# Performance work log

Measured on AMD Instinct MI355X. Metric: run time of the kernel, lower is better.

Reference implementation:

```python
import jax, jax.numpy as jnp
import numpy as np

N_NODES = 100000

def _sage_conv(x, src, dst, w_l, b_l, w_r):
    # PyG SAGEConv (mean aggr): out = lin_l(mean_j x_j) + lin_r(x_i)
    msg = x[src]                                             # [E, d] gather
    agg = jax.ops.segment_sum(msg, dst, num_segments=N_NODES)
    deg = jax.ops.segment_sum(jnp.ones((src.shape[0],), x.dtype), dst,
                              num_segments=N_NODES)
    mean = agg / jnp.maximum(deg, 1.0)[:, None]
    return mean @ w_l.T + b_l + x @ w_r.T


def setup_inputs() -> dict:
    key = jax.random.key(0)
    ks = jax.random.split(key, 9)
    d_in, d_h, d_out = 128, 128, 4
    E = 1600000
    x = jax.random.normal(ks[0], (N_NODES, d_in), dtype=jnp.float32)
    edge_index = jax.random.randint(ks[1], (2, E), 0, N_NODES, dtype=jnp.int32)
    s = lambda k, shp, fan: jax.random.normal(k, shp, jnp.float32) / np.sqrt(fan)
    return {
        "x": x,
        "edge_index": edge_index,
        "w1_l": s(ks[2], (d_h, d_in), d_in),
        "b1_l": jnp.zeros((d_h,), jnp.float32),
        "w1_r": s(ks[3], (d_h, d_in), d_in),
        "w2_l": s(ks[4], (d_h, d_h), d_h),
        "b2_l": jnp.zeros((d_h,), jnp.float32),
        "w2_r": s(ks[5], (d_h, d_h), d_h),
        "w_out": s(ks[6], (d_out, d_h), d_h),
        "b_out": jnp.zeros((d_out,), jnp.float32),
    }


def reference(x, edge_index, w1_l, b1_l, w1_r, w2_l, b2_l, w2_r, w_out, b_out):
    src, dst = edge_index[0], edge_index[1]
    h = jax.nn.relu(_sage_conv(x, src, dst, w1_l, b1_l, w1_r))
    h = jax.nn.relu(_sage_conv(h, src, dst, w2_l, b2_l, w2_r))
    return h @ w_out.T + b_out
```

## Files before the change

### kernel.cpp

```cpp
#include <hip/hip_runtime.h>

constexpr int D = 128;
constexpr int BSHIFT = 10;
constexpr int BNODES = 1 << BSHIFT;
constexpr int NBUCK_MAX = 128;
using short8 = __attribute__((ext_vector_type(8))) short;
using f32x4  = __attribute__((ext_vector_type(4))) float;

__device__ __forceinline__ unsigned rneb(float f) {
    unsigned u = __float_as_uint(f);
    return (u + 0x7fffu + ((u >> 16) & 1u)) >> 16;
}
__device__ __forceinline__ float lo2f(unsigned u) { return __uint_as_float(u << 16); }
__device__ __forceinline__ float hi2f(unsigned u) { return __uint_as_float(u & 0xffff0000u); }

__global__ __launch_bounds__(256) void f32_to_bf16(
    const float* __restrict__ in, unsigned short* __restrict__ out, int n4)
{
    int i = blockIdx.x * 256 + threadIdx.x;
    if (i >= n4) return;
    float4 v = reinterpret_cast<const float4*>(in)[i];
    uint2 o;
    o.x = rneb(v.x) | (rneb(v.y) << 16);
    o.y = rneb(v.z) | (rneb(v.w) << 16);
    reinterpret_cast<uint2*>(out)[i] = o;
}

__global__ __launch_bounds__(256) void pack_w(
    const float* __restrict__ w1l, const float* __restrict__ w1r,
    const float* __restrict__ w2l, const float* __restrict__ w2r,
    unsigned short* __restrict__ wf)
{
    int t = blockIdx.x * 256 + threadIdx.x;
    int m = t >> 11;
    int r = t & 2047;
    int f = r >> 6, lane = r & 63;
    int c = f >> 2, ks = f & 3;
    int col = c * 16 + (lane & 15);
    int k0 = ks * 32 + (lane >> 4) * 8;
    const float* W = (m == 0) ? w1l : (m == 1) ? w1r : (m == 2) ? w2l : w2r;
    unsigned short o[8];
#pragma unroll
    for (int i = 0; i < 8; ++i) o[i] = (unsigned short)rneb(W[col * D + k0 + i]);
    uint4 pk;
    pk.x = o[0] | ((unsigned)o[1] << 16);
    pk.y = o[2] | ((unsigned)o[3] << 16);
    pk.z = o[4] | ((unsigned)o[5] << 16);
    pk.w = o[6] | ((unsigned)o[7] << 16);
    reinterpret_cast<uint4*>(wf)[t] = pk;
}

__global__ __launch_bounds__(256) void hist_kernel(
    const int* __restrict__ dstI, int* __restrict__ degI, int E)
{
    int e = blockIdx.x * 256 + threadIdx.x;
    if (e < E) atomicAdd(&degI[dstI[e]], 1);
}

__global__ __launch_bounds__(256) void scan_blocks(
    const int* __restrict__ degI, int* __restrict__ local,
    int* __restrict__ blocksum, int n)
{
    __shared__ int tmp[256];
    const int t = threadIdx.x;
    const int i = blockIdx.x * 256 + t;
    const int v = (i < n) ? degI[i] : 0;
    tmp[t] = v;
    __syncthreads();
    for (int off = 1; off < 256; off <<= 1) {
        int u = (t >= off) ? tmp[t - off] : 0;
        __syncthreads();
        tmp[t] += u;
        __syncthreads();
    }
    if (i < n) local[i] = tmp[t] - v;
    if (t == 255) blocksum[blockIdx.x] = tmp[255];
}

__global__ __launch_bounds__(1024) void scan_sums(
    int* __restrict__ blocksum, int nb)
{
    __shared__ int tmp[1024];
    const int t = threadIdx.x;
    const int v = (t < nb) ? blocksum[t] : 0;
    tmp[t] = v;
    __syncthreads();
    for (int off = 1; off < 1024; off <<= 1) {
        int u = (t >= off) ? tmp[t - off] : 0;
        __syncthreads();
        tmp[t] += u;
        __syncthreads();
    }
    if (t < nb) blocksum[t] = tmp[t] - v;
}

__global__ __launch_bounds__(256) void finalize_scan(
    const int* __restrict__ local, const int* __restrict__ blocksum,
    int* __restrict__ rowptr, int* __restrict__ gcursor, int n, int E)
{
    const int i = blockIdx.x * 256 + threadIdx.x;
    if (i < n) {
        int r = local[i] + blocksum[blockIdx.x];
        rowptr[i] = r;
        if ((i & (BNODES - 1)) == 0) gcursor[i >> BSHIFT] = r;
    } else if (i == n) {
        rowptr[n] = E;
    }
}

__global__ __launch_bounds__(256) void bin_kernel(
    const int* __restrict__ srcI, const int* __restrict__ dstI,
    int* __restrict__ gcursor, unsigned* __restrict__ binned, int E, int nb)
{
    __shared__ int lhist[NBUCK_MAX];
    __shared__ int lbase[NBUCK_MAX];
    __shared__ int lcnt[NBUCK_MAX];
    const int t = threadIdx.x;
    const int e0 = blockIdx.x * 4096;
    for (int i = t; i < nb; i += 256) { lhist[i] = 0; lcnt[i] = 0; }
    __syncthreads();

    int dcache[16], scache[16];
#pragma unroll
    for (int q = 0; q < 16; ++q) {
        int e = e0 + q * 256 + t;
        int d = (e < E) ? dstI[e] : -1;
        dcache[q] = d;
        scache[q] = (e < E) ? srcI[e] : 0;
        if (d >= 0) atomicAdd(&lhist[d >> BSHIFT], 1);
    }
    __syncthreads();
    for (int b = t; b < nb; b += 256)
        if (lhist[b] > 0) lbase[b] = atomicAdd(&gcursor[b], lhist[b]);
    __syncthreads();
#pragma unroll
    for (int q = 0; q < 16; ++q) {
        int d = dcache[q];
        if (d >= 0) {
            int b = d >> BSHIFT;
            int off = atomicAdd(&lcnt[b], 1);
            binned[lbase[b] + off] =
                (unsigned)scache[q] | ((unsigned)(d & (BNODES - 1)) << 17);
        }
    }
}

__global__ __launch_bounds__(256) void bucket_sort(
    const unsigned* __restrict__ binned, const int* __restrict__ rowptr,
    int* __restrict__ sorted_src, int n)
{
    __shared__ int cursor[BNODES];
    const int node0 = blockIdx.x << BSHIFT;
    const int node1 = min(n, node0 + BNODES);
    for (int i = threadIdx.x; i < node1 - node0; i += 256)
        cursor[i] = rowptr[node0 + i];
    __syncthreads();
    const int ebeg = rowptr[node0];
    const int eend = rowptr[node1];
    for (int e = ebeg + threadIdx.x; e < eend; e += 256) {
        unsigned w = binned[e];
        int pos = atomicAdd(&cursor[w >> 17], 1);
        sorted_src[pos] = (int)(w & 0x1FFFF);
    }
}

__global__ __launch_bounds__(256) void aggregate_bf16(
    const unsigned short* __restrict__ feat, const int* __restrict__ sorted_src,
    const int* __restrict__ rowptr, unsigned short* __restrict__ outb, int n)
{
    const int wid = (blockIdx.x * 256 + threadIdx.x) >> 6;
    if (wid >= n) return;
    const int lane = threadIdx.x & 63;
    const int sub = lane >> 4;
    const int part = lane & 15;
    const int beg = rowptr[wid];
    const int end = rowptr[wid + 1];
    const int deg = end - beg;

    float acc[8];
#pragma unroll
    for (int j = 0; j < 8; ++j) acc[j] = 0.f;

    int e = beg;
    for (; e + 8 <= end; e += 8) {
        const int s0 = sorted_src[e + sub];
        const int s1 = sorted_src[e + 4 + sub];
        const uint4 v0 = *reinterpret_cast<const uint4*>(feat + (size_t)s0 * D + part * 8);
        const uint4 v1 = *reinterpret_cast<const uint4*>(feat + (size_t)s1 * D + part * 8);
        acc[0] += lo2f(v0.x); acc[1] += hi2f(v0.x);
        acc[2] += lo2f(v0.y); acc[3] += hi2f(v0.y);
        acc[4] += lo2f(v0.z); acc[5] += hi2f(v0.z);
        acc[6] += lo2f(v0.w); acc[7] += hi2f(v0.w);
        acc[0] += lo2f(v1.x); acc[1] += hi2f(v1.x);
        acc[2] += lo2f(v1.y); acc[3] += hi2f(v1.y);
        acc[4] += lo2f(v1.z); acc[5] += hi2f(v1.z);
        acc[6] += lo2f(v1.w); acc[7] += hi2f(v1.w);
    }
    if (e + 4 <= end) {
        const int s0 = sorted_src[e + sub];
        const uint4 v0 = *reinterpret_cast<const uint4*>(feat + (size_t)s0 * D + part * 8);
        acc[0] += lo2f(v0.x); acc[1] += hi2f(v0.x);
        acc[2] += lo2f(v0.y); acc[3] += hi2f(v0.y);
        acc[4] += lo2f(v0.z); acc[5] += hi2f(v0.z);
        acc[6] += lo2f(v0.w); acc[7] += hi2f(v0.w);
        e += 4;
    }
    if (e < end) {
        const int ei = e + sub;
        const bool act = ei < end;
        const int s = act ? sorted_src[ei] : sorted_src[beg];
        const float m = act ? 1.f : 0.f;
        const uint4 v = *reinterpret_cast<const uint4*>(feat + (size_t)s * D + part * 8);
        acc[0] += m * lo2f(v.x); acc[1] += m * hi2f(v.x);
        acc[2] += m * lo2f(v.y); acc[3] += m * hi2f(v.y);
        acc[4] += m * lo2f(v.z); acc[5] += m * hi2f(v.z);
        acc[6] += m * lo2f(v.w); acc[7] += m * hi2f(v.w);
    }

#pragma unroll
    for (int j = 0; j < 8; ++j) {
        acc[j] += __shfl_xor(acc[j], 16);
        acc[j] += __shfl_xor(acc[j], 32);
    }

    if (sub == 0) {
        const float inv = (deg > 0) ? 1.0f / (float)deg : 0.f;
        uint4 pk;
        pk.x = rneb(acc[0] * inv) | (rneb(acc[1] * inv) << 16);
        pk.y = rneb(acc[2] * inv) | (rneb(acc[3] * inv) << 16);
        pk.z = rneb(acc[4] * inv) | (rneb(acc[5] * inv) << 16);
        pk.w = rneb(acc[6] * inv) | (rneb(acc[7] * inv) << 16);
        *reinterpret_cast<uint4*>(outb + (size_t)wid * D + part * 8) = pk;
    }
}

__global__ __launch_bounds__(256) void mfma_gemm(
    const unsigned short* __restrict__ aMean, const unsigned short* __restrict__ aSelf,
    const unsigned short* __restrict__ wfL, const unsigned short* __restrict__ wfR,
    const float* __restrict__ bL, unsigned short* __restrict__ outb, int n)
{
    const int lane = threadIdx.x & 63;
    const int wave = threadIdx.x >> 6;
    const int lo = lane & 15, hi = lane >> 4;
    const int row0 = blockIdx.x * 64 + wave * 16;
    int arow = row0 + lo;
    if (arow > n - 1) arow = n - 1;
    const size_t abase = (size_t)arow * D;

    f32x4 acc[8];
#pragma unroll
    for (int c = 0; c < 8; ++c) acc[c] = (f32x4){0.f, 0.f, 0.f, 0.f};

#pragma unroll
    for (int p = 0; p < 2; ++p) {
        const unsigned short* A  = p ? aSelf : aMean;
        const unsigned short* WF = p ? wfR : wfL;
#pragma unroll
        for (int ks = 0; ks < 4; ++ks) {
            short8 af = *reinterpret_cast<const short8*>(A + abase + ks * 32 + hi * 8);
#pragma unroll
            for (int c = 0; c < 8; ++c) {
                short8 bf = *reinterpret_cast<const short8*>(
                    WF + ((((c << 2) | ks) * 64 + lane) << 3));
                acc[c] = __builtin_amdgcn_mfma_f32_16x16x32_bf16(af, bf, acc[c], 0, 0, 0);
            }
        }
    }

#pragma unroll
    for (int c = 0; c < 8; ++c) {
        const int col = (c << 4) | lo;
        const float bias = bL[col];
#pragma unroll
        for (int j = 0; j < 4; ++j) {
            const int row = row0 + (hi << 2) + j;
            if (row < n)
                outb[(size_t)row * D + col] =
                    (unsigned short)rneb(fmaxf(acc[c][j] + bias, 0.f));
        }
    }
}

__global__ __launch_bounds__(256) void out_proj(
    const unsigned short* __restrict__ h2, const float* __restrict__ w_out,
    const float* __restrict__ b_out, float* __restrict__ out, int n)
{
    __shared__ float wsm[4 * D];
    wsm[threadIdx.x] = w_out[threadIdx.x];
    wsm[threadIdx.x + 256] = w_out[threadIdx.x + 256];
    __syncthreads();

    int t = blockIdx.x * 256 + threadIdx.x;
    int i = t >> 5;
    if (i >= n) return;
    int lane = t & 31;

    uint2 u = *reinterpret_cast<const uint2*>(h2 + (size_t)i * D + lane * 4);
    float h0 = lo2f(u.x), h1 = hi2f(u.x), h2v = lo2f(u.y), h3 = hi2f(u.y);
    float p[4];
#pragma unroll
    for (int d = 0; d < 4; ++d) {
        const float* wr = &wsm[d * D + lane * 4];
        p[d] = h0 * wr[0] + h1 * wr[1] + h2v * wr[2] + h3 * wr[3];
    }
#pragma unroll
    for (int off = 16; off > 0; off >>= 1) {
#pragma unroll
        for (int d = 0; d < 4; ++d) p[d] += __shfl_down(p[d], off, 32);
    }
    if (lane == 0) {
        const float4 b = *reinterpret_cast<const float4*>(b_out);
        float4 o;
        o.x = p[0] + b.x; o.y = p[1] + b.y; o.z = p[2] + b.z; o.w = p[3] + b.w;
        *reinterpret_cast<float4*>(out + (size_t)i * 4) = o;
    }
}

extern "C" void kernel_launch(void* const* d_in, const int* in_sizes, int n_in,
                              void* d_out, int out_size, void* d_ws, size_t ws_size,
                              hipStream_t stream)
{
    const float* x    = (const float*)d_in[0];
    const int*   ei   = (const int*)  d_in[1];
    const float* w1l  = (const float*)d_in[2];
    const float* b1l  = (const float*)d_in[3];
    const float* w1r  = (const float*)d_in[4];
    const float* w2l  = (const float*)d_in[5];
    const float* b2l  = (const float*)d_in[6];
    const float* w2r  = (const float*)d_in[7];
    const float* wout = (const float*)d_in[8];
    const float* bout = (const float*)d_in[9];

    const int n = in_sizes[0] / D;
    const int E = in_sizes[1] / 2;
    const int* srcI = ei;
    const int* dstI = ei + E;
    const int nbuck = (n + BNODES - 1) >> BSHIFT;

    auto align256 = [](size_t v) { return (v + 255) & ~(size_t)255; };
    char* base = (char*)d_ws;
    size_t off = 0;
    int* degI = (int*)(base + off);            off = align256(off + sizeof(int) * (size_t)n);
    int* rowptr = (int*)(base + off);          off = align256(off + sizeof(int) * (size_t)(n + 1));
    int* local = (int*)(base + off);           off = align256(off + sizeof(int) * (size_t)n);
    int* blocksum = (int*)(base + off);        off = align256(off + sizeof(int) * 1024);
    int* gcursor = (int*)(base + off);         off = align256(off + sizeof(int) * NBUCK_MAX);
    int* sorted_src = (int*)(base + off);      off = align256(off + sizeof(int) * (size_t)E);
    unsigned* binned = (unsigned*)(base + off); off = align256(off + sizeof(unsigned) * (size_t)E);
    unsigned short* xb = (unsigned short*)(base + off);
    off = align256(off + sizeof(short) * (size_t)n * D);
    unsigned short* bufA = (unsigned short*)(base + off);
    off = align256(off + sizeof(short) * (size_t)n * D);
    unsigned short* bufB = (unsigned short*)(base + off);
    off = align256(off + sizeof(short) * (size_t)n * D);
    unsigned short* wf = (unsigned short*)(base + off);

    hipMemsetAsync(degI, 0, sizeof(int) * (size_t)n, stream);
    const int eblocks = (E + 255) / 256;
    const int nblocks = (n + 255) / 256;
    hist_kernel<<<eblocks, 256, 0, stream>>>(dstI, degI, E);
    scan_blocks<<<nblocks, 256, 0, stream>>>(degI, local, blocksum, n);
    scan_sums<<<1, 1024, 0, stream>>>(blocksum, nblocks);
    finalize_scan<<<(n + 256) / 256, 256, 0, stream>>>(local, blocksum, rowptr,
                                                       gcursor, n, E);
    bin_kernel<<<(E + 4095) / 4096, 256, 0, stream>>>(srcI, dstI, gcursor,
                                                      binned, E, nbuck);
    bucket_sort<<<nbuck, 256, 0, stream>>>(binned, rowptr, sorted_src, n);

    pack_w<<<32, 256, 0, stream>>>(w1l, w1r, w2l, w2r, wf);
    const int n4 = n * (D / 4);
    f32_to_bf16<<<(n4 + 255) / 256, 256, 0, stream>>>(x, xb, n4);

    const int ablocks = (int)(((long long)n * 64 + 255) / 256);
    const int gblocks = (n + 63) / 64;

    aggregate_bf16<<<ablocks, 256, 0, stream>>>(xb, sorted_src, rowptr, bufA, n);
    mfma_gemm<<<gblocks, 256, 0, stream>>>(bufA, xb, wf, wf + 16384, b1l, bufA, n);

    aggregate_bf16<<<ablocks, 256, 0, stream>>>(bufA, sorted_src, rowptr, bufB, n);
    mfma_gemm<<<gblocks, 256, 0, stream>>>(bufB, bufA, wf + 2 * 16384, wf + 3 * 16384, b2l, bufB, n);

    const int oblocks = (int)(((long long)n * 32 + 255) / 256);
    out_proj<<<oblocks, 256, 0, stream>>>(bufB, wout, bout, (float*)d_out, n);
}
```

Before: 425.3 us.

## Replace global degree histogram and scan with per-bucket counting and local CSR build

The CSR construction no longer builds a global per-node degree histogram with global atomics followed by a three-kernel multi-block scan. Instead it counts edges per 512-node bucket using shared-memory histograms, scans the bucket counts in a single block, and has each bucket block compute its per-node histogram, scan and rowptr locally before scattering. Bucket size is halved so a bucket's node histogram fits a 256-thread, two-entries-per-thread scan. This removes the memset, the global atomics on 100k counters and several launches, at the cost of bucket_build reading binned twice.

```diff
diff --git a/kernel.cpp b/kernel.cpp
--- a/kernel.cpp
+++ b/kernel.cpp
@@ -1,9 +1,9 @@
 #include <hip/hip_runtime.h>
 
 constexpr int D = 128;
-constexpr int BSHIFT = 10;
+constexpr int BSHIFT = 9;
 constexpr int BNODES = 1 << BSHIFT;
-constexpr int NBUCK_MAX = 128;
+constexpr int NBUCK_MAX = 256;
 using short8 = __attribute__((ext_vector_type(8))) short;
 using f32x4  = __attribute__((ext_vector_type(4))) float;
 
@@ -50,21 +50,31 @@
     reinterpret_cast<uint4*>(wf)[t] = pk;
 }
 
-__global__ __launch_bounds__(256) void hist_kernel(
-    const int* __restrict__ dstI, int* __restrict__ degI, int E)
-{
-    int e = blockIdx.x * 256 + threadIdx.x;
-    if (e < E) atomicAdd(&degI[dstI[e]], 1);
-}
-
-__global__ __launch_bounds__(256) void scan_blocks(
-    const int* __restrict__ degI, int* __restrict__ local,
-    int* __restrict__ blocksum, int n)
+__global__ __launch_bounds__(256) void bucket_count(
+    const int* __restrict__ dstI, int* __restrict__ bcnt, int E, int nb)
+{
+    __shared__ int lh[NBUCK_MAX];
+    const int t = threadIdx.x;
+    const int e0 = blockIdx.x * 4096;
+    for (int i = t; i < nb; i += 256) lh[i] = 0;
+    __syncthreads();
+#pragma unroll
+    for (int q = 0; q < 16; ++q) {
+        int e = e0 + q * 256 + t;
+        if (e < E) atomicAdd(&lh[dstI[e] >> BSHIFT], 1);
+    }
+    __syncthreads();
+    for (int b = t; b < nb; b += 256)
+        if (lh[b] > 0) atomicAdd(&bcnt[b], lh[b]);
+}
+
+__global__ __launch_bounds__(256) void bucket_scan(
+    const int* __restrict__ bcnt, int* __restrict__ bbase,
+    int* __restrict__ gcursor, int nb)
 {
     __shared__ int tmp[256];
     const int t = threadIdx.x;
-    const int i = blockIdx.x * 256 + t;
-    const int v = (i < n) ? degI[i] : 0;
+    const int v = (t < nb) ? bcnt[t] : 0;
     tmp[t] = v;
     __syncthreads();
     for (int off = 1; off < 256; off <<= 1) {
@@ -73,39 +83,9 @@
         tmp[t] += u;
         __syncthreads();
     }
-    if (i < n) local[i] = tmp[t] - v;
-    if (t == 255) blocksum[blockIdx.x] = tmp[255];
-}
-
-__global__ __launch_bounds__(1024) void scan_sums(
-    int* __restrict__ blocksum, int nb)
-{
-    __shared__ int tmp[1024];
-    const int t = threadIdx.x;
-    const int v = (t < nb) ? blocksum[t] : 0;
-    tmp[t] = v;
-    __syncthreads();
-    for (int off = 1; off < 1024; off <<= 1) {
-        int u = (t >= off) ? tmp[t - off] : 0;
-        __syncthreads();
-        tmp[t] += u;
-        __syncthreads();
-    }
-    if (t < nb) blocksum[t] = tmp[t] - v;
-}
-
-__global__ __launch_bounds__(256) void finalize_scan(
-    const int* __restrict__ local, const int* __restrict__ blocksum,
-    int* __restrict__ rowptr, int* __restrict__ gcursor, int n, int E)
-{
-    const int i = blockIdx.x * 256 + threadIdx.x;
-    if (i < n) {
-        int r = local[i] + blocksum[blockIdx.x];
-        rowptr[i] = r;
-        if ((i & (BNODES - 1)) == 0) gcursor[i >> BSHIFT] = r;
-    } else if (i == n) {
-        rowptr[n] = E;
-    }
+    int excl = tmp[t] - v;
+    if (t < nb) { bbase[t] = excl; gcursor[t] = excl; }
+    if (t == nb - 1) bbase[nb] = excl + v;
 }
 
 __global__ __launch_bounds__(256) void bin_kernel(
@@ -145,21 +125,47 @@
     }
 }
 
-__global__ __launch_bounds__(256) void bucket_sort(
-    const unsigned* __restrict__ binned, const int* __restrict__ rowptr,
-    int* __restrict__ sorted_src, int n)
-{
-    __shared__ int cursor[BNODES];
-    const int node0 = blockIdx.x << BSHIFT;
-    const int node1 = min(n, node0 + BNODES);
-    for (int i = threadIdx.x; i < node1 - node0; i += 256)
-        cursor[i] = rowptr[node0 + i];
-    __syncthreads();
-    const int ebeg = rowptr[node0];
-    const int eend = rowptr[node1];
-    for (int e = ebeg + threadIdx.x; e < eend; e += 256) {
+__global__ __launch_bounds__(256) void bucket_build(
+    const unsigned* __restrict__ binned, const int* __restrict__ bbase,
+    int* __restrict__ rowptr, int* __restrict__ sorted_src, int n, int E)
+{
+    __shared__ int hist[BNODES];
+    __shared__ int cur[BNODES];
+    __shared__ int tmp[256];
+    const int t = threadIdx.x;
+    const int b = blockIdx.x;
+    const int node0 = b << BSHIFT;
+    const int ebeg = bbase[b];
+    const int eend = bbase[b + 1];
+
+    hist[t] = 0; hist[t + 256] = 0;
+    __syncthreads();
+    for (int e = ebeg + t; e < eend; e += 256)
+        atomicAdd(&hist[(binned[e] >> 17) & (BNODES - 1)], 1);
+    __syncthreads();
+
+    const int v0 = hist[2 * t], v1 = hist[2 * t + 1];
+    const int s = v0 + v1;
+    tmp[t] = s;
+    __syncthreads();
+    for (int off = 1; off < 256; off <<= 1) {
+        int u = (t >= off) ? tmp[t - off] : 0;
+        __syncthreads();
+        tmp[t] += u;
+        __syncthreads();
+    }
+    const int pre = ebeg + tmp[t] - s;
+    const int i0 = node0 + 2 * t, i1 = i0 + 1;
+    cur[2 * t] = pre;
+    cur[2 * t + 1] = pre + v0;
+    if (i0 < n) rowptr[i0] = pre;
+    if (i1 < n) rowptr[i1] = pre + v0;
+    if (b == 0 && t == 0) rowptr[n] = E;
+    __syncthreads();
+
+    for (int e = ebeg + t; e < eend; e += 256) {
         unsigned w = binned[e];
-        int pos = atomicAdd(&cursor[w >> 17], 1);
+        int pos = atomicAdd(&cur[(w >> 17) & (BNODES - 1)], 1);
         sorted_src[pos] = (int)(w & 0x1FFFF);
     }
 }
@@ -340,11 +346,10 @@
     auto align256 = [](size_t v) { return (v + 255) & ~(size_t)255; };
     char* base = (char*)d_ws;
     size_t off = 0;
-    int* degI = (int*)(base + off);            off = align256(off + sizeof(int) * (size_t)n);
+    int* bcnt = (int*)(base + off);            off = align256(off + sizeof(int) * NBUCK_MAX);
+    int* bbase = (int*)(base + off);           off = align256(off + sizeof(int) * (NBUCK_MAX + 1));
+    int* gcursor = (int*)(base + off);         off = align256(off + sizeof(int) * NBUCK_MAX);
     int* rowptr = (int*)(base + off);          off = align256(off + sizeof(int) * (size_t)(n + 1));
-    int* local = (int*)(base + off);           off = align256(off + sizeof(int) * (size_t)n);
-    int* blocksum = (int*)(base + off);        off = align256(off + sizeof(int) * 1024);
-    int* gcursor = (int*)(base + off);         off = align256(off + sizeof(int) * NBUCK_MAX);
     int* sorted_src = (int*)(base + off);      off = align256(off + sizeof(int) * (size_t)E);
     unsigned* binned = (unsigned*)(base + off); off = align256(off + sizeof(unsigned) * (size_t)E);
     unsigned short* xb = (unsigned short*)(base + off);
@@ -355,17 +360,12 @@
     off = align256(off + sizeof(short) * (size_t)n * D);
     unsigned short* wf = (unsigned short*)(base + off);
 
-    hipMemsetAsync(degI, 0, sizeof(int) * (size_t)n, stream);
-    const int eblocks = (E + 255) / 256;
-    const int nblocks = (n + 255) / 256;
-    hist_kernel<<<eblocks, 256, 0, stream>>>(dstI, degI, E);
-    scan_blocks<<<nblocks, 256, 0, stream>>>(degI, local, blocksum, n);
-    scan_sums<<<1, 1024, 0, stream>>>(blocksum, nblocks);
-    finalize_scan<<<(n + 256) / 256, 256, 0, stream>>>(local, blocksum, rowptr,
-                                                       gcursor, n, E);
-    bin_kernel<<<(E + 4095) / 4096, 256, 0, stream>>>(srcI, dstI, gcursor,
-                                                      binned, E, nbuck);
-    bucket_sort<<<nbuck, 256, 0, stream>>>(binned, rowptr, sorted_src, n);
+    hipMemsetAsync(bcnt, 0, sizeof(int) * NBUCK_MAX, stream);
+    const int ebblocks = (E + 4095) / 4096;
+    bucket_count<<<ebblocks, 256, 0, stream>>>(dstI, bcnt, E, nbuck);
+    bucket_scan<<<1, 256, 0, stream>>>(bcnt, bbase, gcursor, nbuck);
+    bin_kernel<<<ebblocks, 256, 0, stream>>>(srcI, dstI, gcursor, binned, E, nbuck);
+    bucket_build<<<nbuck, 256, 0, stream>>>(binned, bbase, rowptr, sorted_src, n, E);
 
     pack_w<<<32, 256, 0, stream>>>(w1l, w1r, w2l, w2r, wf);
     const int n4 = n * (D / 4);
```

Result: faster. 358.5 us (-15.7%).
